# Kernel optimization log

Hardware: AMD Instinct MI355X
Metric: run time of the kernel (lower is better)

The kernel has to match this reference:

```python
import jax, jax.numpy as jnp
import numpy as np


def log_g(x):
    # log of g(x) = where(x>=0, x+0.5, sigmoid(x))
    return jnp.where(x >= 0, jnp.log(jnp.maximum(x, 0) + 0.5), -jax.nn.softplus(-x))


def setup_inputs() -> dict:
    key = jax.random.key(0)
    ks = jax.random.split(key, 6)
    B, S, D, H = 4, 4096, 1024, 1024
    x = jax.random.normal(ks[0], (B, S, D), dtype=jnp.float32)
    h0 = jax.random.normal(ks[1], (B, 1, H), dtype=jnp.float32)
    # Linear params (scaled like trained weights to keep activations tame)
    Wz = jax.random.normal(ks[2], (H, D), dtype=jnp.float32) * 0.02
    bz = jax.random.normal(ks[3], (H,), dtype=jnp.float32) * 0.02
    Wh = jax.random.normal(ks[4], (H, D), dtype=jnp.float32) * 0.02
    bh = jax.random.normal(ks[5], (H,), dtype=jnp.float32) * 0.02
    return {"x": x, "h0": h0, "Wz": Wz, "bz": bz, "Wh": Wh, "bh": bh}


def reference(x, h0, Wz, bz, Wh, bh):
    # x: [B,S,D], h0: [B,1,H]
    k = jnp.einsum('bsd,hd->bsh', x, Wz) + bz            # linear_z(x)
    log_z = -jax.nn.softplus(-k)                          # log sigmoid(k)
    log_coeffs = -jax.nn.softplus(k)                      # log (1 - sigmoid(k))
    log_h0 = log_g(h0)                                    # [B,1,H]
    log_tilde_h = log_g(jnp.einsum('bsd,hd->bsh', x, Wh) + bh)
    log_coeffs = jnp.pad(log_coeffs, ((0, 0), (1, 0), (0, 0)))  # prepend zero coeff
    log_values = jnp.concatenate([log_h0, log_z + log_tilde_h], axis=1)  # [B,S+1,H]
    # parallel scan in log space
    a_star = jnp.cumsum(log_coeffs, axis=1)
    log_h = a_star + jax.lax.cumlogsumexp(log_values - a_star, axis=1)
    h = jnp.exp(log_h)
    out = h[:, 1:]                                        # last seq_len steps
    return (out, out[:, -1:])
```

## Files before the change

### kernel.cpp

```cpp
#include <hip/hip_runtime.h>
#include <hip/hip_bf16.h>
#include <stdint.h>

typedef __attribute__((ext_vector_type(4))) float f32x4;
typedef __attribute__((ext_vector_type(8))) short bf16x8;
typedef __attribute__((ext_vector_type(4))) unsigned short u16x4;
typedef __attribute__((ext_vector_type(4))) unsigned int u32x4;

constexpr int cB = 4, cS = 4096, cD = 1024, cH = 1024;
constexpr int cM = cB * cS;
constexpr int cK = cD;
constexpr int NCH = 64;
constexpr int CLEN = cS / NCH;

__device__ __forceinline__ unsigned short f2bf(float f) {
  union { float f; uint32_t u; } v; v.f = f;
  uint32_t r = v.u + 0x7FFFu + ((v.u >> 16) & 1u);
  return (unsigned short)(r >> 16);
}
__device__ __forceinline__ float bf2f(unsigned short h) {
  union { float f; uint32_t u; } v; v.u = ((uint32_t)h) << 16;
  return v.f;
}
__device__ __forceinline__ uint32_t pk2(float lo, float hi) {
  __hip_bfloat162 t = __float22bfloat162_rn(make_float2(lo, hi));
  union { __hip_bfloat162 b; uint32_t u; } v; v.b = t;
  return v.u;
}

__global__ void roundW_kernel(const float* __restrict__ wz, const float* __restrict__ wh,
                              unsigned short* __restrict__ dst) {
  const int nb = (cH * cK) / 1024;
  const int bidx = blockIdx.x;
  const bool second = (bidx >= nb);
  const float* src = second ? wh : wz;
  const int base = ((second ? bidx - nb : bidx) * 256 + threadIdx.x) * 4;
  f32x4 x = *(const f32x4*)(src + base);
  u16x4 h;
#pragma unroll
  for (int j = 0; j < 4; ++j) h[j] = f2bf(x[j]);
  *(u16x4*)(dst + (second ? cH * cK : 0) + base) = h;
}

constexpr int BM = 128, BN = 128, BK = 64;
constexpr int NT = cK / BK;

__global__ __launch_bounds__(256, 2) void gemm_kernel(
    const float* __restrict__ xf,
    const unsigned short* __restrict__ wwh,
    const float* __restrict__ bz, const float* __restrict__ bhv,
    unsigned int* __restrict__ cgbuf,
    float* __restrict__ Pb, float* __restrict__ Qb)
{
  __shared__ unsigned short Ah[BM * BK];
  __shared__ unsigned short Bzb[2][BN * BK];
  __shared__ unsigned short Bhb[2][BN * BK];
  const int tid  = threadIdx.x;
  const int lane = tid & 63;
  const int wv   = tid >> 6;
  const int wr   = wv >> 1, wc = wv & 1;

  const int bid = blockIdx.x;
  const int xcd = bid & 7;
  const int idx = bid >> 3;
  const int mt  = xcd * 16 + (idx >> 3);
  const int nt  = idx & 7;
  const int m0 = mt * BM, n0 = nt * BN;
  const int fr = lane & 15, fq = lane >> 4;

  f32x4 accz[4][4] = {};
  f32x4 acch[4][4] = {};

  const int srow = tid >> 3;
  const int scol = (((tid & 7) ^ (srow & 7)) << 3);

  const float*          gX = xf  + (size_t)m0 * cK;
  const unsigned short* gZ = wwh + (size_t)n0 * cK;
  const unsigned short* gH = wwh + (size_t)(cH + n0) * cK;

#pragma unroll
  for (int r = 0; r < 4; ++r) {
    const int ldsoff = r * 4096 + tid * 16;
    const size_t goff = (size_t)(r * 32 + srow) * cK + scol;
    __builtin_amdgcn_global_load_lds((const __attribute__((address_space(1))) void*)(gZ + goff),
      (__attribute__((address_space(3))) void*)((char*)Bzb[0] + ldsoff), 16, 0, 0);
    __builtin_amdgcn_global_load_lds((const __attribute__((address_space(1))) void*)(gH + goff),
      (__attribute__((address_space(3))) void*)((char*)Bhb[0] + ldsoff), 16, 0, 0);
  }

  for (int kt = 0; kt < NT; ++kt) {
    const int cur = kt & 1, nxt = cur ^ 1;
    const int k0 = kt * BK;
    f32x4 av[8];
#pragma unroll
    for (int r = 0; r < 4; ++r) {
      const size_t goff = (size_t)(r * 32 + srow) * cK + k0 + scol;
      av[2 * r]     = *(const f32x4*)(gX + goff);
      av[2 * r + 1] = *(const f32x4*)(gX + goff + 4);
    }
    if (kt + 1 < NT) {
      const int kn = k0 + BK;
#pragma unroll
      for (int r = 0; r < 4; ++r) {
        const int ldsoff = r * 4096 + tid * 16;
        const size_t goff = (size_t)(r * 32 + srow) * cK + kn + scol;
        __builtin_amdgcn_global_load_lds((const __attribute__((address_space(1))) void*)(gZ + goff),
          (__attribute__((address_space(3))) void*)((char*)Bzb[nxt] + ldsoff), 16, 0, 0);
        __builtin_amdgcn_global_load_lds((const __attribute__((address_space(1))) void*)(gH + goff),
          (__attribute__((address_space(3))) void*)((char*)Bhb[nxt] + ldsoff), 16, 0, 0);
      }
    }
    asm volatile("s_waitcnt vmcnt(8)" ::: "memory");
#pragma unroll
    for (int r = 0; r < 4; ++r) {
      u32x4 apk;
      apk[0] = pk2(av[2 * r][0], av[2 * r][1]);
      apk[1] = pk2(av[2 * r][2], av[2 * r][3]);
      apk[2] = pk2(av[2 * r + 1][0], av[2 * r + 1][1]);
      apk[3] = pk2(av[2 * r + 1][2], av[2 * r + 1][3]);
      *(u32x4*)((char*)Ah + r * 4096 + tid * 16) = apk;
    }
    asm volatile("s_waitcnt lgkmcnt(0)\n\ts_barrier" ::: "memory");
#pragma unroll
    for (int kk = 0; kk < BK / 32; ++kk) {
      bf16x8 fa[4], fz[4], fh[4];
#pragma unroll
      for (int i = 0; i < 4; ++i) {
        const int ar = wr * 64 + i * 16 + fr;
        const int ca = (kk * 64 + fq * 16) ^ ((ar & 7) << 4);
        fa[i] = *(const bf16x8*)((const char*)Ah + ar * 128 + ca);
        const int br = wc * 64 + i * 16 + fr;
        const int cb = (kk * 64 + fq * 16) ^ ((br & 7) << 4);
        fz[i] = *(const bf16x8*)((const char*)Bzb[cur] + br * 128 + cb);
        fh[i] = *(const bf16x8*)((const char*)Bhb[cur] + br * 128 + cb);
      }
#pragma unroll
      for (int i = 0; i < 4; ++i)
#pragma unroll
        for (int j = 0; j < 4; ++j) {
          accz[i][j] = __builtin_amdgcn_mfma_f32_16x16x32_bf16(fa[i], fz[j], accz[i][j], 0, 0, 0);
          acch[i][j] = __builtin_amdgcn_mfma_f32_16x16x32_bf16(fa[i], fh[j], acch[i][j], 0, 0, 0);
        }
    }
    asm volatile("s_barrier" ::: "memory");
  }

  const int b  = mt >> 5;
  const int ch = (mt & 31) * 2 + wr;
#pragma unroll
  for (int j = 0; j < 4; ++j) {
    const int n = n0 + wc * 64 + j * 16 + fr;
    const float bz_n = bz[n];
    const float bh_n = bhv[n];
    float psg[4], qsg[4];
#pragma unroll
    for (int i = 0; i < 4; ++i) {
      float p = 1.0f, q = 0.0f;
#pragma unroll
      for (int rg = 0; rg < 4; ++rg) {
        const int m = m0 + wr * 64 + i * 16 + fq * 4 + rg;
        const float kv = accz[i][j][rg] + bz_n;
        const float av2 = acch[i][j][rg] + bh_n;
        const float c = __builtin_amdgcn_rcpf(1.0f + __expf(kv));
        const float g = (av2 >= 0.0f) ? (av2 + 0.5f)
                                      : __builtin_amdgcn_rcpf(1.0f + __expf(-av2));
        cgbuf[(size_t)m * cH + n] = pk2(c, g);
        q = c * q + (1.0f - c) * g;
        p = c * p;
      }
      float pp = __shfl_xor(p, 16), qq = __shfl_xor(q, 16);
      if (fq & 1) { q = q + p * qq; } else { q = qq + pp * q; }
      p = p * pp;
      pp = __shfl_xor(p, 32); qq = __shfl_xor(q, 32);
      if (fq & 2) { q = q + p * qq; } else { q = qq + pp * q; }
      p = p * pp;
      psg[i] = p; qsg[i] = q;
    }
    float P = psg[0], Q = qsg[0];
#pragma unroll
    for (int i = 1; i < 4; ++i) { Q = qsg[i] + psg[i] * Q; P = psg[i] * P; }
    if (fq == 0) {
      const size_t o = ((size_t)b * NCH + ch) * cH + n;
      Pb[o] = P; Qb[o] = Q;
    }
  }
}

__global__ void scan_prefix_kernel(const float* __restrict__ h0,
                                   const float* __restrict__ Pb, const float* __restrict__ Qb,
                                   float* __restrict__ hin) {
  const int wid  = (blockIdx.x * blockDim.x + threadIdx.x) >> 6;
  const int lane = threadIdx.x & 63;
  const int b = wid >> 10, h = wid & 1023;
  const size_t o = ((size_t)b * NCH + lane) * cH + h;
  float P = Pb[o], Q = Qb[o];
#pragma unroll
  for (int off = 1; off < 64; off <<= 1) {
    float Po = __shfl_up(P, off), Qo = __shfl_up(Q, off);
    if (lane >= off) { Q = P * Qo + Q; P = P * Po; }
  }
  float Pe = __shfl_up(P, 1), Qe = __shfl_up(Q, 1);
  if (lane == 0) { Pe = 1.0f; Qe = 0.0f; }
  const float x = h0[b * cH + h];
  const float h0g = (x >= 0.0f) ? (x + 0.5f) : (1.0f / (1.0f + expf(-x)));
  hin[o] = Pe * h0g + Qe;
}

__global__ void scan_write_kernel(const unsigned int* __restrict__ cg,
                                  const float* __restrict__ hin, float* __restrict__ out) {
  const int bc = blockIdx.x;
  const int b = bc / NCH, ch = bc % NCH;
  const int h4 = threadIdx.x * 4;
  f32x4 hc = *(const f32x4*)(hin + ((size_t)b * NCH + ch) * cH + h4);
  size_t base = ((size_t)b * cS + (size_t)ch * CLEN) * cH + h4;
#pragma unroll 4
  for (int i = 0; i < CLEN; ++i) {
    u32x4 v = *(const u32x4*)(cg + base + (size_t)i * cH);
#pragma unroll
    for (int j = 0; j < 4; ++j) {
      const float c = bf2f((unsigned short)(v[j] & 0xFFFFu));
      const float g = bf2f((unsigned short)(v[j] >> 16));
      hc[j] = c * hc[j] + (1.0f - c) * g;
    }
    *(f32x4*)(out + base + (size_t)i * cH) = hc;
  }
  if (ch == NCH - 1) {
    *(f32x4*)(out + (size_t)cM * cH + (size_t)b * cH + h4) = hc;
  }
}

extern "C" void kernel_launch(void* const* d_in, const int* in_sizes, int n_in,
                              void* d_out, int out_size, void* d_ws, size_t ws_size,
                              hipStream_t stream) {
  const float* x   = (const float*)d_in[0];
  const float* h0  = (const float*)d_in[1];
  const float* Wz  = (const float*)d_in[2];
  const float* bz  = (const float*)d_in[3];
  const float* Wh  = (const float*)d_in[4];
  const float* bh  = (const float*)d_in[5];

  char* ws = (char*)d_ws;
  unsigned short* wwh  = (unsigned short*)(ws + (((size_t)32) << 20));
  unsigned int*   cgbuf= (unsigned int*)(ws + (((size_t)40) << 20));
  float* Pb   = (float*)(ws + (((size_t)104) << 20));
  float* Qb   = (float*)(ws + (((size_t)105) << 20));
  float* hin  = (float*)(ws + (((size_t)106) << 20));
  float* out  = (float*)d_out;

  roundW_kernel<<<2 * cH * cK / 1024, 256, 0, stream>>>(Wz, Wh, wwh);
  gemm_kernel<<<(cM / BM) * (cH / BN), 256, 0, stream>>>(x, wwh, bz, bh, cgbuf, Pb, Qb);
  scan_prefix_kernel<<<cB * cH * 64 / 256, 256, 0, stream>>>(h0, Pb, Qb, hin);
  scan_write_kernel<<<cB * NCH, 256, 0, stream>>>(cgbuf, hin, out);
}
```

Measured before the change: 117.7 us.

## Load A fragments directly from global into registers, dropping A LDS staging

The A (x) tile is no longer converted to bf16 and staged through shared memory. Each wave loads its own MFMA fragment rows of fp32 x straight from global memory, converts them to bf16 in registers, and splits the two K-halves so the second half's loads overlap the first half's MFMAs. This removes the A LDS writes and reads and frees LDS, which may help occupancy. In exchange, the two waves that share the same rows (wc=0/1) both fetch that x data, doubling A global/L2 traffic, and the per-lane loads are less coalesced.

After: 188.9 us. 1.61x slower.

```diff
diff --git a/kernel.cpp b/kernel.cpp
--- a/kernel.cpp
+++ b/kernel.cpp
@@ -52,7 +52,6 @@
     unsigned int* __restrict__ cgbuf,
     float* __restrict__ Pb, float* __restrict__ Qb)
 {
-  __shared__ unsigned short Ah[BM * BK];
   __shared__ unsigned short Bzb[2][BN * BK];
   __shared__ unsigned short Bhb[2][BN * BK];
   const int tid  = threadIdx.x;
@@ -74,9 +73,9 @@
   const int srow = tid >> 3;
   const int scol = (((tid & 7) ^ (srow & 7)) << 3);
 
-  const float*          gX = xf  + (size_t)m0 * cK;
   const unsigned short* gZ = wwh + (size_t)n0 * cK;
   const unsigned short* gH = wwh + (size_t)(cH + n0) * cK;
+  const float* gA = xf + (size_t)(m0 + wr * 64 + fr) * cK;
 
 #pragma unroll
   for (int r = 0; r < 4; ++r) {
@@ -91,12 +90,57 @@
   for (int kt = 0; kt < NT; ++kt) {
     const int cur = kt & 1, nxt = cur ^ 1;
     const int k0 = kt * BK;
-    f32x4 av[8];
-#pragma unroll
-    for (int r = 0; r < 4; ++r) {
-      const size_t goff = (size_t)(r * 32 + srow) * cK + k0 + scol;
-      av[2 * r]     = *(const f32x4*)(gX + goff);
-      av[2 * r + 1] = *(const f32x4*)(gX + goff + 4);
+    f32x4 a0[4], a1[4];
+#pragma unroll
+    for (int i = 0; i < 4; ++i) {
+      const float* p = gA + (size_t)(i * 16) * cK + k0 + fq * 8;
+      a0[i] = *(const f32x4*)p;
+      a1[i] = *(const f32x4*)(p + 4);
+    }
+    asm volatile("s_waitcnt vmcnt(8)" ::: "memory");
+    asm volatile("s_barrier" ::: "memory");
+    bf16x8 fa0[4];
+#pragma unroll
+    for (int i = 0; i < 4; ++i) {
+      union { u32x4 u; bf16x8 b; } cv;
+      cv.u[0] = pk2(a0[i][0], a0[i][1]);
+      cv.u[1] = pk2(a0[i][2], a0[i][3]);
+      cv.u[2] = pk2(a1[i][0], a1[i][1]);
+      cv.u[3] = pk2(a1[i][2], a1[i][3]);
+      fa0[i] = cv.b;
+    }
+#pragma unroll
+    for (int i = 0; i < 4; ++i) {
+      const float* p = gA + (size_t)(i * 16) * cK + k0 + 32 + fq * 8;
+      a0[i] = *(const f32x4*)p;
+      a1[i] = *(const f32x4*)(p + 4);
+    }
+    {
+      bf16x8 fz[4], fh[4];
+#pragma unroll
+      for (int i = 0; i < 4; ++i) {
+        const int br = wc * 64 + i * 16 + fr;
+        const int cb = (fq * 16) ^ ((br & 7) << 4);
+        fz[i] = *(const bf16x8*)((const char*)Bzb[cur] + br * 128 + cb);
+        fh[i] = *(const bf16x8*)((const char*)Bhb[cur] + br * 128 + cb);
+      }
+#pragma unroll
+      for (int i = 0; i < 4; ++i)
+#pragma unroll
+        for (int j = 0; j < 4; ++j) {
+          accz[i][j] = __builtin_amdgcn_mfma_f32_16x16x32_bf16(fa0[i], fz[j], accz[i][j], 0, 0, 0);
+          acch[i][j] = __builtin_amdgcn_mfma_f32_16x16x32_bf16(fa0[i], fh[j], acch[i][j], 0, 0, 0);
+        }
+    }
+    bf16x8 fa1[4];
+#pragma unroll
+    for (int i = 0; i < 4; ++i) {
+      union { u32x4 u; bf16x8 b; } cv;
+      cv.u[0] = pk2(a0[i][0], a0[i][1]);
+      cv.u[1] = pk2(a0[i][2], a0[i][3]);
+      cv.u[2] = pk2(a1[i][0], a1[i][1]);
+      cv.u[3] = pk2(a1[i][2], a1[i][3]);
+      fa1[i] = cv.b;
     }
     if (kt + 1 < NT) {
       const int kn = k0 + BK;
@@ -110,27 +154,12 @@
           (__attribute__((address_space(3))) void*)((char*)Bhb[nxt] + ldsoff), 16, 0, 0);
       }
     }
-    asm volatile("s_waitcnt vmcnt(8)" ::: "memory");
-#pragma unroll
-    for (int r = 0; r < 4; ++r) {
-      u32x4 apk;
-      apk[0] = pk2(av[2 * r][0], av[2 * r][1]);
-      apk[1] = pk2(av[2 * r][2], av[2 * r][3]);
-      apk[2] = pk2(av[2 * r + 1][0], av[2 * r + 1][1]);
-      apk[3] = pk2(av[2 * r + 1][2], av[2 * r + 1][3]);
-      *(u32x4*)((char*)Ah + r * 4096 + tid * 16) = apk;
-    }
-    asm volatile("s_waitcnt lgkmcnt(0)\n\ts_barrier" ::: "memory");
-#pragma unroll
-    for (int kk = 0; kk < BK / 32; ++kk) {
-      bf16x8 fa[4], fz[4], fh[4];
+    {
+      bf16x8 fz[4], fh[4];
 #pragma unroll
       for (int i = 0; i < 4; ++i) {
-        const int ar = wr * 64 + i * 16 + fr;
-        const int ca = (kk * 64 + fq * 16) ^ ((ar & 7) << 4);
-        fa[i] = *(const bf16x8*)((const char*)Ah + ar * 128 + ca);
         const int br = wc * 64 + i * 16 + fr;
-        const int cb = (kk * 64 + fq * 16) ^ ((br & 7) << 4);
+        const int cb = (64 + fq * 16) ^ ((br & 7) << 4);
         fz[i] = *(const bf16x8*)((const char*)Bzb[cur] + br * 128 + cb);
         fh[i] = *(const bf16x8*)((const char*)Bhb[cur] + br * 128 + cb);
       }
@@ -138,8 +167,8 @@
       for (int i = 0; i < 4; ++i)
 #pragma unroll
         for (int j = 0; j < 4; ++j) {
-          accz[i][j] = __builtin_amdgcn_mfma_f32_16x16x32_bf16(fa[i], fz[j], accz[i][j], 0, 0, 0);
-          acch[i][j] = __builtin_amdgcn_mfma_f32_16x16x32_bf16(fa[i], fh[j], acch[i][j], 0, 0, 0);
+          accz[i][j] = __builtin_amdgcn_mfma_f32_16x16x32_bf16(fa1[i], fz[j], accz[i][j], 0, 0, 0);
+          acch[i][j] = __builtin_amdgcn_mfma_f32_16x16x32_bf16(fa1[i], fh[j], acch[i][j], 0, 0, 0);
         }
     }
     asm volatile("s_barrier" ::: "memory");
```
